# Kernel optimization log

Measured on AMD Instinct MI355X. Metric: run time of the kernel, lower is better.

Reference implementation:

```python
import jax, jax.numpy as jnp
import numpy as np
from jax import lax

B, T, C = 2, 2048, 2048
H, KV = 16, 4
D = C // H          # 128 head_dim
EPS = 1e-5
THETA = 10000.0
NEG = -1e9


def setup_inputs() -> dict:
    key = jax.random.key(0)
    ks = jax.random.split(key, 12)
    x = jax.random.normal(ks[0], (B, T, C), dtype=jnp.float32)
    s_in = 1.0 / np.sqrt(C)
    s_attn = 1.0 / np.sqrt(C)
    Wq = jax.random.normal(ks[1], (C, H * D), jnp.float32) * s_in
    Wk = jax.random.normal(ks[2], (C, KV * D), jnp.float32) * s_in
    Wv = jax.random.normal(ks[3], (C, KV * D), jnp.float32) * s_in
    Wo = jax.random.normal(ks[4], (H * D, C), jnp.float32) * s_attn
    bq = jnp.zeros((H * D,), jnp.float32)
    bk = jnp.zeros((KV * D,), jnp.float32)
    bv = jnp.zeros((KV * D,), jnp.float32)
    bo = jnp.zeros((C,), jnp.float32)
    qn_w = jnp.ones((D,), jnp.float32)
    kn_w = jnp.ones((D,), jnp.float32)
    # rotary tables: freqs_cis[t, j] = exp(i * t * theta^(-2j/D))
    inv_freq = 1.0 / (THETA ** (jnp.arange(0, D, 2, dtype=jnp.float32) / D))  # [D/2]
    angles = jnp.arange(T, dtype=jnp.float32)[:, None] * inv_freq[None, :]    # [T, D/2]
    freqs_cos = jnp.cos(angles)
    freqs_sin = jnp.sin(angles)
    # additive causal mask [1,1,T,T]
    causal = jnp.tril(jnp.ones((T, T), dtype=bool))
    mask = jnp.where(causal, 0.0, NEG).astype(jnp.float32)[None, None]
    return {"x": x, "Wq": Wq, "bq": bq, "Wk": Wk, "bk": bk, "Wv": Wv, "bv": bv,
            "Wo": Wo, "bo": bo, "qn_w": qn_w, "kn_w": kn_w,
            "freqs_cos": freqs_cos, "freqs_sin": freqs_sin, "mask": mask}


def _rmsnorm(h, w):
    var = jnp.mean(jnp.square(h), axis=-1, keepdims=True)
    return h * jax.lax.rsqrt(var + EPS) * w


def _rope(h, cos, sin):
    # h: [B,T,n,D]; cos/sin: [T, D/2] -> broadcast [1,T,1,D/2]
    hr = h.reshape(*h.shape[:-1], D // 2, 2)
    a, b = hr[..., 0], hr[..., 1]
    c = cos[None, :, None, :]
    s = sin[None, :, None, :]
    out = jnp.stack([a * c - b * s, a * s + b * c], axis=-1)
    return out.reshape(h.shape)


def reference(x, Wq, bq, Wk, bk, Wv, bv, Wo, bo, qn_w, kn_w, freqs_cos, freqs_sin, mask):
    q = (x @ Wq + bq).reshape(B, T, H, D)
    k = (x @ Wk + bk).reshape(B, T, KV, D)
    v = (x @ Wv + bv).reshape(B, T, KV, D)
    q = _rmsnorm(q, qn_w)
    k = _rmsnorm(k, kn_w)
    q = _rope(q, freqs_cos, freqs_sin)
    k = _rope(k, freqs_cos, freqs_sin)
    # GQA: repeat kv heads (interleaved, matching jnp.repeat on axis=2)
    k = jnp.repeat(k, H // KV, axis=2)
    v = jnp.repeat(v, H // KV, axis=2)
    q, k, v = (jnp.swapaxes(t, 1, 2) for t in (q, k, v))  # [B,H,T,D]
    scale = 1.0 / jnp.sqrt(jnp.float32(D))
    scores = jnp.einsum('bhid,bhjd->bhij', q, k) * scale + mask
    scores = scores - lax.stop_gradient(jnp.max(scores, axis=-1, keepdims=True))
    w = jnp.exp(scores)
    w = w / jnp.sum(w, axis=-1, keepdims=True)
    out = jnp.einsum('bhij,bhjd->bhid', w, v)
    out = jnp.swapaxes(out, 1, 2).reshape(B, T, H * D)
    return out @ Wo + bo
```

## Files before the change

kernel.cpp:

```cpp
#include <hip/hip_runtime.h>

typedef __bf16 bf16_t;
typedef __bf16 bf16x8 __attribute__((ext_vector_type(8)));
typedef __bf16 bf16x4 __attribute__((ext_vector_type(4)));
typedef float f32x4 __attribute__((ext_vector_type(4)));
typedef unsigned int u32;

#define B_    2
#define T_    2048
#define C_    2048
#define H_    16
#define KV_   4
#define D_    128
#define NT_   4096
#define NQKV_ 3072

__device__ __forceinline__ void gload16(const void* g, void* l) {
  __builtin_amdgcn_global_load_lds((const __attribute__((address_space(1))) u32*)g,
                                   (__attribute__((address_space(3))) u32*)l, 16, 0, 0);
}

__global__ __launch_bounds__(256) void k_convert(const float* __restrict__ x,
                                                 bf16_t* __restrict__ y, int n4) {
  int i = blockIdx.x * 256 + threadIdx.x;
  if (i >= n4) return;
  float4 v = ((const float4*)x)[i];
  bf16x4 o;
  o[0] = (bf16_t)v.x; o[1] = (bf16_t)v.y; o[2] = (bf16_t)v.z; o[3] = (bf16_t)v.w;
  ((bf16x4*)y)[i] = o;
}

__global__ __launch_bounds__(256) void k_transpose(const float* __restrict__ W,
                                                   bf16_t* __restrict__ Wt, int K, int N) {
  __shared__ float tile[32][33];
  int n0 = blockIdx.x * 32, k0 = blockIdx.y * 32;
  int tx = threadIdx.x & 31, ty = threadIdx.x >> 5;
#pragma unroll
  for (int r = 0; r < 32; r += 8)
    tile[ty + r][tx] = W[(size_t)(k0 + ty + r) * N + n0 + tx];
  __syncthreads();
#pragma unroll
  for (int r = 0; r < 32; r += 8)
    Wt[(size_t)(n0 + ty + r) * K + k0 + tx] = (bf16_t)tile[tx][ty + r];
}

__global__ void k_bias(const float* __restrict__ bq, const float* __restrict__ bk,
                       const float* __restrict__ bv, float* __restrict__ o) {
  int i = blockIdx.x * 256 + threadIdx.x;
  if (i < 2048) o[i] = bq[i];
  else if (i < 2560) o[i] = bk[i - 2048];
  else if (i < 3072) o[i] = bv[i - 2560];
}

__global__ __launch_bounds__(512, 2) void k_gemm(const bf16_t* __restrict__ A,
                                                 const bf16_t* __restrict__ Wt,
                                                 const float* __restrict__ bias,
                                                 float* __restrict__ Cout, int NTOT) {
  constexpr int K = 2048;
  constexpr int NK = K / 64;
  __shared__ __align__(16) bf16_t Asr[3][256 * 64];
  __shared__ __align__(16) bf16_t Bsr[3][128 * 64];
  const int tid = threadIdx.x;
  const int lane = tid & 63, w = tid >> 6;
  const int c = lane & 15, g = lane >> 4;
  const int wr = w >> 1, wc = w & 1;
  const int m0 = blockIdx.y * 256, n0 = blockIdx.x * 128;

  int arow[4], asc[4], brow[2], bsc[2];
#pragma unroll
  for (int i = 0; i < 4; ++i) {
    const int ck = i * 512 + w * 64 + lane;
    arow[i] = ck >> 3; asc[i] = ((ck & 7) ^ ((ck >> 3) & 7)) * 8;
  }
#pragma unroll
  for (int j = 0; j < 2; ++j) {
    const int ck = j * 512 + w * 64 + lane;
    brow[j] = ck >> 3; bsc[j] = ((ck & 7) ^ ((ck >> 3) & 7)) * 8;
  }
  const int swz0 = ((0 * 4 + g) ^ (c & 7)) * 8;
  const int swz1 = ((1 * 4 + g) ^ (c & 7)) * 8;
  const int aro = (wr * 64 + c) * 64;
  const int bro = (wc * 64 + c) * 64;

  const f32x4 fz = {0.f, 0.f, 0.f, 0.f};
  f32x4 acc[4][4];
#pragma unroll
  for (int m = 0; m < 4; ++m)
#pragma unroll
    for (int n = 0; n < 4; ++n) acc[m][n] = fz;

  auto stageA2 = [&](int ts, int sl, int i0) {
    const int k0 = ts * 64;
#pragma unroll
    for (int i = i0; i < i0 + 2; ++i)
      gload16(A + (size_t)(m0 + arow[i]) * K + k0 + asc[i],
              Asr[sl] + (i * 512 + w * 64) * 8);
  };
  auto stageB1 = [&](int ts, int sl, int j) {
    const int k0 = ts * 64;
    gload16(Wt + (size_t)(n0 + brow[j]) * K + k0 + bsc[j],
            Bsr[sl] + (j * 512 + w * 64) * 8);
  };

  stageA2(0, 0, 0); stageA2(0, 0, 2); stageB1(0, 0, 0); stageB1(0, 0, 1);
  stageA2(1, 1, 0); stageA2(1, 1, 2); stageB1(1, 1, 0); stageB1(1, 1, 1);
  asm volatile("s_waitcnt vmcnt(6)" ::: "memory");
  __builtin_amdgcn_s_barrier();

  int slot = 0;
#pragma unroll 1
  for (int t = 0; t < NK; ++t) {
    const int sl2 = (slot >= 1) ? slot - 1 : 2;
    const int ts = (t + 2 < NK) ? t + 2 : NK - 1;
    const bf16_t* Ap = Asr[slot];
    const bf16_t* Bp = Bsr[slot];

    bf16x8 af[4][2], b01[2][2];
#pragma unroll
    for (int m = 0; m < 4; ++m) {
      af[m][0] = *(const bf16x8*)(Ap + aro + m * 1024 + swz0);
      af[m][1] = *(const bf16x8*)(Ap + aro + m * 1024 + swz1);
    }
#pragma unroll
    for (int n = 0; n < 2; ++n) {
      b01[n][0] = *(const bf16x8*)(Bp + bro + n * 1024 + swz0);
      b01[n][1] = *(const bf16x8*)(Bp + bro + n * 1024 + swz1);
    }
    stageA2(ts, sl2, 0); stageB1(ts, sl2, 0);
    __builtin_amdgcn_s_barrier();
    asm volatile("s_waitcnt lgkmcnt(0)" ::: "memory");
    __builtin_amdgcn_sched_barrier(0);
    __builtin_amdgcn_s_setprio(1);
#pragma unroll
    for (int m = 0; m < 4; ++m)
#pragma unroll
      for (int n = 0; n < 2; ++n) {
        acc[m][n] = __builtin_amdgcn_mfma_f32_16x16x32_bf16(af[m][0], b01[n][0], acc[m][n], 0, 0, 0);
        acc[m][n] = __builtin_amdgcn_mfma_f32_16x16x32_bf16(af[m][1], b01[n][1], acc[m][n], 0, 0, 0);
      }
    __builtin_amdgcn_s_setprio(0);
    __builtin_amdgcn_s_barrier();

    bf16x8 b23[2][2];
#pragma unroll
    for (int n = 0; n < 2; ++n) {
      b23[n][0] = *(const bf16x8*)(Bp + bro + (n + 2) * 1024 + swz0);
      b23[n][1] = *(const bf16x8*)(Bp + bro + (n + 2) * 1024 + swz1);
    }
    stageA2(ts, sl2, 2); stageB1(ts, sl2, 1);
    __builtin_amdgcn_s_barrier();
    asm volatile("s_waitcnt lgkmcnt(0)" ::: "memory");
    __builtin_amdgcn_sched_barrier(0);
    __builtin_amdgcn_s_setprio(1);
#pragma unroll
    for (int m = 0; m < 4; ++m)
#pragma unroll
      for (int n = 0; n < 2; ++n) {
        acc[m][n + 2] = __builtin_amdgcn_mfma_f32_16x16x32_bf16(af[m][0], b23[n][0], acc[m][n + 2], 0, 0, 0);
        acc[m][n + 2] = __builtin_amdgcn_mfma_f32_16x16x32_bf16(af[m][1], b23[n][1], acc[m][n + 2], 0, 0, 0);
      }
    __builtin_amdgcn_s_setprio(0);
    asm volatile("s_waitcnt vmcnt(6)" ::: "memory");
    __builtin_amdgcn_s_barrier();
    __builtin_amdgcn_sched_barrier(0);
    slot = (slot == 2) ? 0 : slot + 1;
  }

#pragma unroll
  for (int n = 0; n < 4; ++n) {
    const int col = n0 + wc * 64 + n * 16 + c;
    const float bn = bias[col];
#pragma unroll
    for (int m = 0; m < 4; ++m) {
      const int row = m0 + wr * 64 + m * 16 + g * 4;
#pragma unroll
      for (int r = 0; r < 4; ++r)
        Cout[(size_t)(row + r) * NTOT + col] = acc[m][n][r] + bn;
    }
  }
}

__global__ __launch_bounds__(256) void k_rmsrope(const float* __restrict__ qkv,
                                                 const float* __restrict__ qw,
                                                 const float* __restrict__ kw,
                                                 const float* __restrict__ fc,
                                                 const float* __restrict__ fs,
                                                 bf16_t* __restrict__ Qb,
                                                 bf16_t* __restrict__ Kb,
                                                 bf16_t* __restrict__ Vt) {
  const int bt = blockIdx.x;
  const int u = blockIdx.y * 4 + (threadIdx.x >> 6);
  const int lane = threadIdx.x & 63;
  const int b = bt >> 11, t = bt & (T_ - 1);
  int off;
  if (u < 16) off = u * 128;
  else if (u < 20) off = 2048 + (u - 16) * 128;
  else off = 2560 + (u - 20) * 128;
  const float2 ab = *(const float2*)(qkv + (size_t)bt * NQKV_ + off + 2 * lane);
  const float a = ab.x, bv_ = ab.y;
  if (u < 20) {
    float ssq = a * a + bv_ * bv_;
#pragma unroll
    for (int o = 32; o; o >>= 1) ssq += __shfl_xor(ssq, o, 64);
    const float r = rsqrtf(ssq * (1.0f / 128.0f) + 1e-5f);
    const float* wgt = (u < 16) ? qw : kw;
    const float a2 = a * r * wgt[2 * lane];
    const float b2 = bv_ * r * wgt[2 * lane + 1];
    const float cs = fc[t * 64 + lane], sn = fs[t * 64 + lane];
    const float o0 = a2 * cs - b2 * sn;
    const float o1 = a2 * sn + b2 * cs;
    const u32 pk = ((u32)__builtin_bit_cast(unsigned short, (bf16_t)o1) << 16) |
                   (u32)__builtin_bit_cast(unsigned short, (bf16_t)o0);
    if (u < 16)
      *(u32*)(Qb + ((size_t)(b * H_ + u) * T_ + t) * D_ + 2 * lane) = pk;
    else
      *(u32*)(Kb + ((size_t)(b * KV_ + (u - 16)) * T_ + t) * D_ + 2 * lane) = pk;
  } else {
    const int kv = u - 20;
    bf16_t* vp = Vt + (size_t)(b * KV_ + kv) * D_ * T_;
    vp[(size_t)(2 * lane) * T_ + t] = (bf16_t)a;
    vp[(size_t)(2 * lane + 1) * T_ + t] = (bf16_t)bv_;
  }
}

__global__ __launch_bounds__(256) void k_attn(const bf16_t* __restrict__ Q,
                                              const bf16_t* __restrict__ K,
                                              const bf16_t* __restrict__ Vt,
                                              bf16_t* __restrict__ Aout) {
  const int pi = blockIdx.x, h = blockIdx.y, b = blockIdx.z;
  const int tid = threadIdx.x, w = tid >> 6, lane = tid & 63;
  const int c = lane & 15, g = lane >> 4;
  const int kv = h >> 2;

  __shared__ __align__(16) bf16_t Ks[2][64 * 128];
  __shared__ __align__(16) bf16_t Vs[2][128 * 64];
  __shared__ __align__(16) bf16_t P[4][16][72];

  const bf16_t* Kp = K + (size_t)(b * KV_ + kv) * T_ * D_;
  const bf16_t* Vp = Vt + (size_t)(b * KV_ + kv) * D_ * T_;
  const float scale = 0.08838834764831845f;
  const f32x4 fz = {0.f, 0.f, 0.f, 0.f};

  int krow[4], kcol[4], vrow[4], vcol[4];
#pragma unroll
  for (int i = 0; i < 4; ++i) {
    const int ck = i * 256 + w * 64 + lane;
    krow[i] = ck >> 4;
    kcol[i] = (((ck & 15) ^ ((ck >> 4) & 7)) * 8);
    vrow[i] = ck >> 3;
    vcol[i] = (((ck & 7) ^ ((ck >> 3) & 7)) * 8);
  }

  auto stage = [&](int k0, int buf) {
#pragma unroll
    for (int i = 0; i < 4; ++i) {
      const int lu = (i * 256 + w * 64) * 8;
      gload16(Kp + (size_t)(k0 + krow[i]) * D_ + kcol[i], Ks[buf] + lu);
      gload16(Vp + (size_t)vrow[i] * T_ + k0 + vcol[i], Vs[buf] + lu);
    }
  };

#pragma unroll 1
  for (int ph = 0; ph < 2; ++ph) {
    const int qt = (ph == 0) ? pi : 31 - pi;
    const int q0 = qt * 64;
    const int nkt = qt + 1;

    const bf16_t* Qp = Q + ((size_t)(b * H_ + h) * T_ + q0 + w * 16 + c) * D_;
    bf16x8 qf[4];
#pragma unroll
    for (int ks = 0; ks < 4; ++ks) qf[ks] = *(const bf16x8*)(Qp + ks * 32 + g * 8);

    f32x4 o[8];
#pragma unroll
    for (int d = 0; d < 8; ++d) o[d] = fz;
    float mr[4], lr[4];
#pragma unroll
    for (int r = 0; r < 4; ++r) { mr[r] = -__builtin_inff(); lr[r] = 0.f; }

    if (ph == 1) __syncthreads();
    stage(0, 0);
    int cur = 0;

#pragma unroll 1
    for (int kt = 0; kt < nkt; ++kt) {
      __syncthreads();
      if (kt + 1 < nkt) stage((kt + 1) * 64, cur ^ 1);
      const int k0 = kt * 64;
      const char* Kc = (const char*)(Ks[cur]);
      const char* Vc = (const char*)(Vs[cur]);
      const int sw = (c & 7) << 4;

      f32x4 s[4];
#pragma unroll
      for (int jf = 0; jf < 4; ++jf) {
        f32x4 sj = fz;
#pragma unroll
        for (int ks = 0; ks < 4; ++ks) {
          bf16x8 kf = *(const bf16x8*)(Kc + (jf * 16 + c) * 256 + (((ks * 4 + g) * 16) ^ sw));
          sj = __builtin_amdgcn_mfma_f32_16x16x32_bf16(qf[ks], kf, sj, 0, 0, 0);
        }
        s[jf] = sj;
      }
      if (kt == qt) {
#pragma unroll
        for (int jf = 0; jf < 4; ++jf) {
          const int key = k0 + jf * 16 + c;
#pragma unroll
          for (int r = 0; r < 4; ++r) {
            const int qr = q0 + w * 16 + g * 4 + r;
            s[jf][r] = (key <= qr) ? s[jf][r] * scale : -1e30f;
          }
        }
      } else {
#pragma unroll
        for (int jf = 0; jf < 4; ++jf)
#pragma unroll
          for (int r = 0; r < 4; ++r) s[jf][r] *= scale;
      }
      float tm[4];
#pragma unroll
      for (int r = 0; r < 4; ++r) {
        tm[r] = fmaxf(fmaxf(s[0][r], s[1][r]), fmaxf(s[2][r], s[3][r]));
        tm[r] = fmaxf(tm[r], __shfl_xor(tm[r], 1, 64));
        tm[r] = fmaxf(tm[r], __shfl_xor(tm[r], 2, 64));
        tm[r] = fmaxf(tm[r], __shfl_xor(tm[r], 4, 64));
        tm[r] = fmaxf(tm[r], __shfl_xor(tm[r], 8, 64));
      }
      float al[4], rs[4];
#pragma unroll
      for (int r = 0; r < 4; ++r) {
        const float nm = fmaxf(mr[r], tm[r]);
        al[r] = __expf(mr[r] - nm);
        mr[r] = nm;
        rs[r] = 0.f;
      }
#pragma unroll
      for (int jf = 0; jf < 4; ++jf)
#pragma unroll
        for (int r = 0; r < 4; ++r) {
          const float p = __expf(s[jf][r] - mr[r]);
          s[jf][r] = p;
          rs[r] += p;
        }
#pragma unroll
      for (int r = 0; r < 4; ++r) {
        rs[r] += __shfl_xor(rs[r], 1, 64);
        rs[r] += __shfl_xor(rs[r], 2, 64);
        rs[r] += __shfl_xor(rs[r], 4, 64);
        rs[r] += __shfl_xor(rs[r], 8, 64);
        lr[r] = lr[r] * al[r] + rs[r];
      }
#pragma unroll
      for (int d = 0; d < 8; ++d)
#pragma unroll
        for (int r = 0; r < 4; ++r) o[d][r] *= al[r];
#pragma unroll
      for (int jf = 0; jf < 4; ++jf)
#pragma unroll
        for (int r = 0; r < 4; ++r)
          P[w][g * 4 + r][jf * 16 + c] = (bf16_t)s[jf][r];
#pragma unroll
      for (int ks2 = 0; ks2 < 2; ++ks2) {
        const bf16x8 pa = *(const bf16x8*)&P[w][c][ks2 * 32 + g * 8];
#pragma unroll
        for (int d = 0; d < 8; ++d) {
          const bf16x8 vf = *(const bf16x8*)(Vc + (d * 16 + c) * 128 + (((ks2 * 4 + g) * 16) ^ sw));
          o[d] = __builtin_amdgcn_mfma_f32_16x16x32_bf16(pa, vf, o[d], 0, 0, 0);
        }
      }
      cur ^= 1;
    }

    float inv[4];
#pragma unroll
    for (int r = 0; r < 4; ++r) inv[r] = 1.0f / lr[r];
#pragma unroll
    for (int d = 0; d < 8; ++d)
#pragma unroll
      for (int r = 0; r < 4; ++r)
        Aout[(size_t)(b * T_ + q0 + w * 16 + g * 4 + r) * C_ + h * D_ + d * 16 + c] =
            (bf16_t)(o[d][r] * inv[r]);
  }
}

extern "C" void kernel_launch(void* const* d_in, const int* in_sizes, int n_in,
                              void* d_out, int out_size, void* d_ws, size_t ws_size,
                              hipStream_t stream) {
  const float* x  = (const float*)d_in[0];
  const float* Wq = (const float*)d_in[1];
  const float* bq = (const float*)d_in[2];
  const float* Wk = (const float*)d_in[3];
  const float* bk = (const float*)d_in[4];
  const float* Wv = (const float*)d_in[5];
  const float* bv = (const float*)d_in[6];
  const float* Wo = (const float*)d_in[7];
  const float* bo = (const float*)d_in[8];
  const float* qw = (const float*)d_in[9];
  const float* kw = (const float*)d_in[10];
  const float* fc = (const float*)d_in[11];
  const float* fs = (const float*)d_in[12];
  float* out = (float*)d_out;

  char* p = (char*)d_ws;
  bf16_t* xb   = (bf16_t*)p; p += (size_t)NT_ * C_ * 2;
  bf16_t* Wqkv = (bf16_t*)p; p += (size_t)NQKV_ * C_ * 2;
  bf16_t* Wot  = (bf16_t*)p; p += (size_t)C_ * C_ * 2;
  float*  qkv  = (float*)p;  p += (size_t)NT_ * NQKV_ * 4;
  bf16_t* Qb   = (bf16_t*)p; p += (size_t)B_ * H_ * T_ * D_ * 2;
  bf16_t* Kb   = (bf16_t*)p; p += (size_t)B_ * KV_ * T_ * D_ * 2;
  bf16_t* Vt   = (bf16_t*)p; p += (size_t)B_ * KV_ * T_ * D_ * 2;
  float*  bqkv = (float*)p;  p += NQKV_ * 4;
  bf16_t* attn = xb;

  k_convert<<<NT_ * C_ / 4 / 256, 256, 0, stream>>>(x, xb, NT_ * C_ / 4);
  k_transpose<<<dim3(64, 64), 256, 0, stream>>>(Wq, Wqkv, 2048, 2048);
  k_transpose<<<dim3(16, 64), 256, 0, stream>>>(Wk, Wqkv + (size_t)2048 * 2048, 2048, 512);
  k_transpose<<<dim3(16, 64), 256, 0, stream>>>(Wv, Wqkv + (size_t)2560 * 2048, 2048, 512);
  k_transpose<<<dim3(64, 64), 256, 0, stream>>>(Wo, Wot, 2048, 2048);
  k_bias<<<12, 256, 0, stream>>>(bq, bk, bv, bqkv);
  k_gemm<<<dim3(NQKV_ / 128, NT_ / 256), 512, 0, stream>>>(xb, Wqkv, bqkv, qkv, NQKV_);
  k_rmsrope<<<dim3(NT_, 6), 256, 0, stream>>>(qkv, qw, kw, fc, fs, Qb, Kb, Vt);
  k_attn<<<dim3(16, H_, B_), 256, 0, stream>>>(Qb, Kb, Vt, attn);
  k_gemm<<<dim3(C_ / 128, NT_ / 256), 512, 0, stream>>>(attn, Wot, bo, out, C_);
}
```

Measured before the change: 384.9 us.

## Rewrite attention with 32x32 MFMA, split-K waves, XCD-aware mapping

The attention kernel is restructured to use 512-thread blocks of 8 waves with 128-row query tiles. Pairs of waves split each key tile and merge their partial softmax states through shared memory. It switches to 32x32x16 bf16 MFMA with K as the A operand, so P stays in registers via v_permlane32_swap instead of a shared-memory round trip. The softmax scale and log2(e) are folded into Q in the rmsnorm/rope kernel, so the kernel can use exp2f. Block ids are remapped so that heads sharing a KV head land on the same XCD. This adds a cross-wave merge step with extra LDS (~64KB Os) and a sync, and it relies on a gfx950-specific instruction.

```diff
diff --git a/kernel.cpp b/kernel.cpp
--- a/kernel.cpp
+++ b/kernel.cpp
@@ -4,6 +4,7 @@
 typedef __bf16 bf16x8 __attribute__((ext_vector_type(8)));
 typedef __bf16 bf16x4 __attribute__((ext_vector_type(4)));
 typedef float f32x4 __attribute__((ext_vector_type(4)));
+typedef float f32x16 __attribute__((ext_vector_type(16)));
 typedef unsigned int u32;
 
 #define B_    2
@@ -18,6 +19,14 @@
 __device__ __forceinline__ void gload16(const void* g, void* l) {
   __builtin_amdgcn_global_load_lds((const __attribute__((address_space(1))) u32*)g,
                                    (__attribute__((address_space(3))) u32*)l, 16, 0, 0);
+}
+
+__device__ __forceinline__ u32 pack2(float lo, float hi) {
+  return ((u32)__builtin_bit_cast(unsigned short, (bf16_t)hi) << 16) |
+         (u32)__builtin_bit_cast(unsigned short, (bf16_t)lo);
+}
+__device__ __forceinline__ void plswap(u32& x, u32& y) {
+  asm volatile("v_permlane32_swap_b32 %0, %1" : "+v"(x), "+v"(y));
 }
 
 __global__ __launch_bounds__(256) void k_convert(const float* __restrict__ x,
@@ -207,8 +216,12 @@
     const float a2 = a * r * wgt[2 * lane];
     const float b2 = bv_ * r * wgt[2 * lane + 1];
     const float cs = fc[t * 64 + lane], sn = fs[t * 64 + lane];
-    const float o0 = a2 * cs - b2 * sn;
-    const float o1 = a2 * sn + b2 * cs;
+    float o0 = a2 * cs - b2 * sn;
+    float o1 = a2 * sn + b2 * cs;
+    if (u < 16) {
+      const float SCLQ = 0.08838834764831845f * 1.4426950408889634f;
+      o0 *= SCLQ; o1 *= SCLQ;
+    }
     const u32 pk = ((u32)__builtin_bit_cast(unsigned short, (bf16_t)o1) << 16) |
                    (u32)__builtin_bit_cast(unsigned short, (bf16_t)o0);
     if (u < 16)
@@ -223,60 +236,60 @@
   }
 }
 
-__global__ __launch_bounds__(256) void k_attn(const bf16_t* __restrict__ Q,
-                                              const bf16_t* __restrict__ K,
-                                              const bf16_t* __restrict__ Vt,
-                                              bf16_t* __restrict__ Aout) {
-  const int pi = blockIdx.x, h = blockIdx.y, b = blockIdx.z;
-  const int tid = threadIdx.x, w = tid >> 6, lane = tid & 63;
-  const int c = lane & 15, g = lane >> 4;
-  const int kv = h >> 2;
+__global__ __launch_bounds__(512, 2) void k_attn(const bf16_t* __restrict__ Q,
+                                                 const bf16_t* __restrict__ K,
+                                                 const bf16_t* __restrict__ Vt,
+                                                 bf16_t* __restrict__ Aout) {
+  const int wg = blockIdx.x;
+  const int xcd = wg & 7, idx = wg >> 3;
+  const int b = xcd >> 2, kvh = xcd & 3;
+  const int h = kvh * 4 + (idx & 3);
+  const int pi = idx >> 2;
+
+  const int tid = threadIdx.x, lane = tid & 63, w = tid >> 6;
+  const int c5 = lane & 31, g = lane >> 5;
+  const int wq = w >> 1, wk = w & 1;
 
   __shared__ __align__(16) bf16_t Ks[2][64 * 128];
   __shared__ __align__(16) bf16_t Vs[2][128 * 64];
-  __shared__ __align__(16) bf16_t P[4][16][72];
-
-  const bf16_t* Kp = K + (size_t)(b * KV_ + kv) * T_ * D_;
-  const bf16_t* Vp = Vt + (size_t)(b * KV_ + kv) * D_ * T_;
-  const float scale = 0.08838834764831845f;
-  const f32x4 fz = {0.f, 0.f, 0.f, 0.f};
-
-  int krow[4], kcol[4], vrow[4], vcol[4];
-#pragma unroll
-  for (int i = 0; i < 4; ++i) {
-    const int ck = i * 256 + w * 64 + lane;
-    krow[i] = ck >> 4;
-    kcol[i] = (((ck & 15) ^ ((ck >> 4) & 7)) * 8);
-    vrow[i] = ck >> 3;
-    vcol[i] = (((ck & 7) ^ ((ck >> 3) & 7)) * 8);
-  }
-
+  __shared__ float Os[4][64][64];
+  __shared__ float Ms[4][64], Ls[4][64];
+
+  const bf16_t* Kp = K + (size_t)(b * KV_ + kvh) * T_ * D_;
+  const bf16_t* Vp = Vt + (size_t)(b * KV_ + kvh) * D_ * T_;
+
+  int kr[2], kc[2], vr[2], vc[2];
+#pragma unroll
+  for (int i = 0; i < 2; ++i) {
+    const int ck = i * 512 + tid;
+    kr[i] = ck >> 4; kc[i] = ((ck & 15) ^ (kr[i] & 15)) * 8;
+    vr[i] = ck >> 3; vc[i] = ((ck & 7) ^ (vr[i] & 7)) * 8;
+  }
   auto stage = [&](int k0, int buf) {
 #pragma unroll
-    for (int i = 0; i < 4; ++i) {
-      const int lu = (i * 256 + w * 64) * 8;
-      gload16(Kp + (size_t)(k0 + krow[i]) * D_ + kcol[i], Ks[buf] + lu);
-      gload16(Vp + (size_t)vrow[i] * T_ + k0 + vcol[i], Vs[buf] + lu);
+    for (int i = 0; i < 2; ++i) {
+      gload16(Kp + (size_t)(k0 + kr[i]) * D_ + kc[i], Ks[buf] + (i * 512 + w * 64) * 8);
+      gload16(Vp + (size_t)vr[i] * T_ + k0 + vc[i], Vs[buf] + (i * 512 + w * 64) * 8);
     }
   };
 
 #pragma unroll 1
   for (int ph = 0; ph < 2; ++ph) {
-    const int qt = (ph == 0) ? pi : 31 - pi;
-    const int q0 = qt * 64;
-    const int nkt = qt + 1;
-
-    const bf16_t* Qp = Q + ((size_t)(b * H_ + h) * T_ + q0 + w * 16 + c) * D_;
-    bf16x8 qf[4];
-#pragma unroll
-    for (int ks = 0; ks < 4; ++ks) qf[ks] = *(const bf16x8*)(Qp + ks * 32 + g * 8);
-
-    f32x4 o[8];
-#pragma unroll
-    for (int d = 0; d < 8; ++d) o[d] = fz;
-    float mr[4], lr[4];
-#pragma unroll
-    for (int r = 0; r < 4; ++r) { mr[r] = -__builtin_inff(); lr[r] = 0.f; }
+    const int qt = ph ? 15 - pi : pi;
+    const int q0 = qt * 128;
+    const int nkt = 2 * (qt + 1);
+    const int qrow = q0 + wq * 32 + c5;
+    const bf16_t* Qp = Q + ((size_t)(b * H_ + h) * T_ + qrow) * D_;
+    bf16x8 qf[8];
+#pragma unroll
+    for (int t = 0; t < 8; ++t) qf[t] = *(const bf16x8*)(Qp + t * 16 + g * 8);
+
+    f32x16 o[4];
+#pragma unroll
+    for (int d = 0; d < 4; ++d)
+#pragma unroll
+      for (int r = 0; r < 16; ++r) o[d][r] = 0.f;
+    float mr = 0.f, lr = 0.f;
 
     if (ph == 1) __syncthreads();
     stage(0, 0);
@@ -286,101 +299,96 @@
     for (int kt = 0; kt < nkt; ++kt) {
       __syncthreads();
       if (kt + 1 < nkt) stage((kt + 1) * 64, cur ^ 1);
-      const int k0 = kt * 64;
-      const char* Kc = (const char*)(Ks[cur]);
-      const char* Vc = (const char*)(Vs[cur]);
-      const int sw = (c & 7) << 4;
-
-      f32x4 s[4];
-#pragma unroll
-      for (int jf = 0; jf < 4; ++jf) {
-        f32x4 sj = fz;
-#pragma unroll
-        for (int ks = 0; ks < 4; ++ks) {
-          bf16x8 kf = *(const bf16x8*)(Kc + (jf * 16 + c) * 256 + (((ks * 4 + g) * 16) ^ sw));
-          sj = __builtin_amdgcn_mfma_f32_16x16x32_bf16(qf[ks], kf, sj, 0, 0, 0);
+      const int kbase = kt * 64 + wk * 32;
+      if (kbase <= q0 + wq * 32 + 31) {
+        const bf16_t* Kc = Ks[cur];
+        const bf16_t* Vc = Vs[cur];
+        const int sw16 = c5 & 15, sw8 = c5 & 7;
+        const int krowoff = (wk * 32 + c5) * 128;
+
+        f32x16 s;
+#pragma unroll
+        for (int r = 0; r < 16; ++r) s[r] = 0.f;
+#pragma unroll
+        for (int t = 0; t < 8; ++t) {
+          bf16x8 kf = *(const bf16x8*)(Kc + krowoff + (((2 * t + g) ^ sw16) * 8));
+          s = __builtin_amdgcn_mfma_f32_32x32x16_bf16(kf, qf[t], s, 0, 0, 0);
         }
-        s[jf] = sj;
-      }
-      if (kt == qt) {
-#pragma unroll
-        for (int jf = 0; jf < 4; ++jf) {
-          const int key = k0 + jf * 16 + c;
-#pragma unroll
-          for (int r = 0; r < 4; ++r) {
-            const int qr = q0 + w * 16 + g * 4 + r;
-            s[jf][r] = (key <= qr) ? s[jf][r] * scale : -1e30f;
+        if (kbase + 31 > q0 + wq * 32) {
+#pragma unroll
+          for (int r = 0; r < 16; ++r) {
+            const int key = kbase + (r & 3) + 8 * (r >> 2) + 4 * g;
+            s[r] = (key <= qrow) ? s[r] : -1e30f;
           }
         }
-      } else {
-#pragma unroll
-        for (int jf = 0; jf < 4; ++jf)
-#pragma unroll
-          for (int r = 0; r < 4; ++r) s[jf][r] *= scale;
-      }
-      float tm[4];
-#pragma unroll
-      for (int r = 0; r < 4; ++r) {
-        tm[r] = fmaxf(fmaxf(s[0][r], s[1][r]), fmaxf(s[2][r], s[3][r]));
-        tm[r] = fmaxf(tm[r], __shfl_xor(tm[r], 1, 64));
-        tm[r] = fmaxf(tm[r], __shfl_xor(tm[r], 2, 64));
-        tm[r] = fmaxf(tm[r], __shfl_xor(tm[r], 4, 64));
-        tm[r] = fmaxf(tm[r], __shfl_xor(tm[r], 8, 64));
-      }
-      float al[4], rs[4];
-#pragma unroll
-      for (int r = 0; r < 4; ++r) {
-        const float nm = fmaxf(mr[r], tm[r]);
-        al[r] = __expf(mr[r] - nm);
-        mr[r] = nm;
-        rs[r] = 0.f;
-      }
-#pragma unroll
-      for (int jf = 0; jf < 4; ++jf)
-#pragma unroll
-        for (int r = 0; r < 4; ++r) {
-          const float p = __expf(s[jf][r] - mr[r]);
-          s[jf][r] = p;
-          rs[r] += p;
+        float tm = s[0];
+#pragma unroll
+        for (int r = 1; r < 16; ++r) tm = fmaxf(tm, s[r]);
+        tm = fmaxf(tm, __shfl_xor(tm, 32, 64));
+        const float nm = fmaxf(mr, tm);
+        const float al = exp2f(mr - nm);
+        mr = nm;
+        float p[16];
+        float rs = 0.f;
+#pragma unroll
+        for (int r = 0; r < 16; ++r) { p[r] = exp2f(s[r] - nm); rs += p[r]; }
+        rs += __shfl_xor(rs, 32, 64);
+        lr = lr * al + rs;
+#pragma unroll
+        for (int d = 0; d < 4; ++d)
+#pragma unroll
+          for (int r = 0; r < 16; ++r) o[d][r] *= al;
+
+        u32 pk01[4], pk23[4];
+#pragma unroll
+        for (int b2 = 0; b2 < 4; ++b2) {
+          pk01[b2] = pack2(p[4 * b2], p[4 * b2 + 1]);
+          pk23[b2] = pack2(p[4 * b2 + 2], p[4 * b2 + 3]);
         }
 #pragma unroll
-      for (int r = 0; r < 4; ++r) {
-        rs[r] += __shfl_xor(rs[r], 1, 64);
-        rs[r] += __shfl_xor(rs[r], 2, 64);
-        rs[r] += __shfl_xor(rs[r], 4, 64);
-        rs[r] += __shfl_xor(rs[r], 8, 64);
-        lr[r] = lr[r] * al[r] + rs[r];
-      }
-#pragma unroll
-      for (int d = 0; d < 8; ++d)
-#pragma unroll
-        for (int r = 0; r < 4; ++r) o[d][r] *= al[r];
-#pragma unroll
-      for (int jf = 0; jf < 4; ++jf)
-#pragma unroll
-        for (int r = 0; r < 4; ++r)
-          P[w][g * 4 + r][jf * 16 + c] = (bf16_t)s[jf][r];
-#pragma unroll
-      for (int ks2 = 0; ks2 < 2; ++ks2) {
-        const bf16x8 pa = *(const bf16x8*)&P[w][c][ks2 * 32 + g * 8];
-#pragma unroll
-        for (int d = 0; d < 8; ++d) {
-          const bf16x8 vf = *(const bf16x8*)(Vc + (d * 16 + c) * 128 + (((ks2 * 4 + g) * 16) ^ sw));
-          o[d] = __builtin_amdgcn_mfma_f32_16x16x32_bf16(pa, vf, o[d], 0, 0, 0);
+        for (int i = 0; i < 2; ++i) {
+          u32 a0 = pk01[2 * i], b0 = pk01[2 * i + 1];
+          u32 a1 = pk23[2 * i], b1 = pk23[2 * i + 1];
+          plswap(a0, b0); plswap(a1, b1);
+          union { u32 u[4]; bf16x8 v; } pu;
+          pu.u[0] = a0; pu.u[1] = a1; pu.u[2] = b0; pu.u[3] = b1;
+#pragma unroll
+          for (int d = 0; d < 4; ++d) {
+            bf16x8 vf = *(const bf16x8*)(Vc + (d * 32 + c5) * 64 +
+                                         (((wk * 4 + 2 * i + g) ^ sw8) * 8));
+            o[d] = __builtin_amdgcn_mfma_f32_32x32x16_bf16(vf, pu.v, o[d], 0, 0, 0);
+          }
         }
       }
       cur ^= 1;
     }
 
-    float inv[4];
-#pragma unroll
-    for (int r = 0; r < 4; ++r) inv[r] = 1.0f / lr[r];
-#pragma unroll
-    for (int d = 0; d < 8; ++d)
-#pragma unroll
-      for (int r = 0; r < 4; ++r)
-        Aout[(size_t)(b * T_ + q0 + w * 16 + g * 4 + r) * C_ + h * D_ + d * 16 + c] =
-            (bf16_t)(o[d][r] * inv[r]);
+    if (wk == 1) {
+#pragma unroll
+      for (int d = 0; d < 4; ++d)
+#pragma unroll
+        for (int r = 0; r < 16; ++r) Os[wq][d * 16 + r][lane] = o[d][r];
+      Ms[wq][lane] = mr; Ls[wq][lane] = lr;
+    }
+    __syncthreads();
+    if (wk == 0) {
+      const float m1 = Ms[wq][lane], l1 = Ls[wq][lane];
+      const float nm = fmaxf(mr, m1);
+      const float a0 = exp2f(mr - nm), a1 = exp2f(m1 - nm);
+      const float inv = 1.0f / (lr * a0 + l1 * a1);
+      bf16_t* op = Aout + (size_t)(b * T_ + qrow) * C_ + h * D_;
+#pragma unroll
+      for (int d = 0; d < 4; ++d)
+#pragma unroll
+        for (int b2 = 0; b2 < 4; ++b2) {
+          bf16x4 pkv;
+#pragma unroll
+          for (int r3 = 0; r3 < 4; ++r3)
+            pkv[r3] = (bf16_t)((o[d][4 * b2 + r3] * a0 +
+                                Os[wq][d * 16 + 4 * b2 + r3][lane] * a1) * inv);
+          *(bf16x4*)(op + d * 32 + 8 * b2 + 4 * g) = pkv;
+        }
+    }
   }
 }
 
@@ -421,6 +429,6 @@
   k_bias<<<12, 256, 0, stream>>>(bq, bk, bv, bqkv);
   k_gemm<<<dim3(NQKV_ / 128, NT_ / 256), 512, 0, stream>>>(xb, Wqkv, bqkv, qkv, NQKV_);
   k_rmsrope<<<dim3(NT_, 6), 256, 0, stream>>>(qkv, qw, kw, fc, fs, Qb, Kb, Vt);
-  k_attn<<<dim3(16, H_, B_), 256, 0, stream>>>(Qb, Kb, Vt, attn);
+  k_attn<<<256, 512, 0, stream>>>(Qb, Kb, Vt, attn);
   k_gemm<<<dim3(C_ / 128, NT_ / 256), 512, 0, stream>>>(attn, Wot, bo, out, C_);
 }
```

Result: faster. 363.7 us (-5.5%).
